# Kernel tuning notes

Measured on AMD Instinct MI355X. Metric: run time of the kernel, lower is better.

## Reference

```python
import jax, jax.numpy as jnp
import numpy as np

B, W, C, N = 2, 2048, 512, 8
K = C // N                      # 64
HALF = K * (K + 1) // 2 - K     # strict upper-triangle count
EPS = 1e-5


def _layernorm(x, gamma, beta):
    mu = jnp.mean(x, axis=-1, keepdims=True)
    var = jnp.mean(jnp.square(x - mu), axis=-1, keepdims=True)
    return (x - mu) * jax.lax.rsqrt(var + EPS) * gamma + beta


def _build_metric(halves, diagonals):
    # symmetric per-head metric: strict upper triangle from `halves`,
    # mirrored, diagonal overwritten by `diagonals` (diag of m+m^T is 0).
    iu0, iu1 = np.triu_indices(K, k=1)
    m = jnp.zeros((N, K, K), dtype=halves.dtype).at[:, iu0, iu1].set(halves)
    m = m + jnp.swapaxes(m, -1, -2)
    d = np.arange(K)
    return m.at[:, d, d].set(diagonals)


def setup_inputs() -> dict:
    key = jax.random.key(0)
    ks = jax.random.split(key, 9)
    return {
        "x1": jax.random.normal(ks[0], (B, W, C), jnp.float32),
        "x2": jax.random.normal(ks[1], (B, W, C), jnp.float32),
        "gamma": jnp.ones((C,), jnp.float32),
        "beta": jnp.zeros((C,), jnp.float32),
        "proj_nck": jax.random.normal(ks[2], (N, C, K), jnp.float32) * (C ** -0.5),
        "halves": jax.random.normal(ks[3], (N, HALF), jnp.float32) * 0.05,
        "diagonals": jax.random.normal(ks[4], (N, K), jnp.float32) * 0.05,
        "W_mixer": jax.random.normal(ks[5], (C, C), jnp.float32) * 0.02,
        "b_mixer": jnp.zeros((C,), jnp.float32),
    }


def reference(x1, x2, gamma, beta, proj_nck, halves, diagonals, W_mixer, b_mixer):
    x1n = _layernorm(x1, gamma, beta)
    x2n = _layernorm(x2, gamma, beta)
    metric_nkk = _build_metric(halves, diagonals)

    # per-head projections (same projection used for both sequences)
    p1_bnwk = jnp.einsum("bwc,nck->bnwk", x1n, proj_nck)
    p2_bnwk = jnp.einsum("bwc,nck->bnwk", x2n, proj_nck)

    # bilinear metric scores  Q . M . K^T  -> [B, N, W, W]
    dots_bnww = jnp.einsum("bnwk,nkj,bnvj->bnwv", p1_bnwk, metric_nkk, p2_bnwk)

    # NOTE: the original computes a scaled/masked softmax of dots_bnww but
    # never uses it for the output; the value mix uses the RAW dot products.
    # We omit the dead softmax — output math is identical.

    nudged_bnwk = jnp.einsum("bnwv,bnvk->bnwk", dots_bnww, p1_bnwk)
    nudged_bwc = jnp.transpose(nudged_bnwk, (0, 2, 1, 3)).reshape(x1.shape[0], x1.shape[1], C)
    return nudged_bwc @ W_mixer.T + b_mixer
```

## Files before the change

kernel.cpp:

```cpp
#include <hip/hip_runtime.h>

typedef unsigned short u16;
typedef __attribute__((ext_vector_type(8))) short short8;
typedef __attribute__((ext_vector_type(4))) float f32x4;

#define HALFN 2016

__device__ __forceinline__ u16 f2b_rn(float x) {
    union { float f; unsigned u; } v; v.f = x;
    unsigned r = v.u + 0x7FFFu + ((v.u >> 16) & 1u);
    return (u16)(r >> 16);
}

__device__ __forceinline__ void gll16(const void* g, void* s) {
    __builtin_amdgcn_global_load_lds(
        (const __attribute__((address_space(1))) unsigned int*)g,
        (__attribute__((address_space(3))) unsigned int*)s, 16, 0, 0);
}

__global__ __launch_bounds__(256) void ln_prep(const float* __restrict__ x1,
                                               const float* __restrict__ x2,
                                               const float* __restrict__ gamma,
                                               const float* __restrict__ beta,
                                               const float* __restrict__ proj,
                                               u16* __restrict__ Xh,
                                               u16* __restrict__ Pwh,
                                               float* __restrict__ S) {
    const int bid = blockIdx.x, t = threadIdx.x;

    if (bid < 2048) {
        const int wv = t >> 6, lane = t & 63;
        const int row = bid * 4 + wv;
        const float* src = (row < 4096) ? (x1 + (size_t)row * 512)
                                        : (x2 + (size_t)(row - 4096) * 512);
        float4 v0 = *(const float4*)&src[lane * 4];
        float4 v1 = *(const float4*)&src[256 + lane * 4];
        float s  = v0.x + v0.y + v0.z + v0.w + v1.x + v1.y + v1.z + v1.w;
        float sq = v0.x * v0.x + v0.y * v0.y + v0.z * v0.z + v0.w * v0.w +
                   v1.x * v1.x + v1.y * v1.y + v1.z * v1.z + v1.w * v1.w;
        #pragma unroll
        for (int off = 32; off > 0; off >>= 1) {
            s  += __shfl_down(s, off);
            sq += __shfl_down(sq, off);
        }
        s  = __shfl(s, 0);
        sq = __shfl(sq, 0);
        float mu  = s * (1.0f / 512.0f);
        float var = sq * (1.0f / 512.0f) - mu * mu;
        float rs  = rsqrtf(var + 1e-5f);
        float4 g0 = *(const float4*)&gamma[lane * 4];
        float4 g1 = *(const float4*)&gamma[256 + lane * 4];
        float4 b0 = *(const float4*)&beta[lane * 4];
        float4 b1 = *(const float4*)&beta[256 + lane * 4];
        ushort4 h0, h1;
        h0.x = f2b_rn((v0.x - mu) * rs * g0.x + b0.x);
        h0.y = f2b_rn((v0.y - mu) * rs * g0.y + b0.y);
        h0.z = f2b_rn((v0.z - mu) * rs * g0.z + b0.z);
        h0.w = f2b_rn((v0.w - mu) * rs * g0.w + b0.w);
        h1.x = f2b_rn((v1.x - mu) * rs * g1.x + b1.x);
        h1.y = f2b_rn((v1.y - mu) * rs * g1.y + b1.y);
        h1.z = f2b_rn((v1.z - mu) * rs * g1.z + b1.z);
        h1.w = f2b_rn((v1.w - mu) * rs * g1.w + b1.w);
        *(ushort4*)&Xh[(size_t)row * 512 + lane * 4] = h0;
        *(ushort4*)&Xh[(size_t)row * 512 + 256 + lane * 4] = h1;
    } else if (bid < 2112) {
        __shared__ float tile[64][65];
        const int id = bid - 2048;
        const int n = id >> 3, c0 = (id & 7) * 64;
        #pragma unroll
        for (int i = 0; i < 4; i++) {
            int flat = i * 256 + t;
            int c = flat >> 4, k4 = (flat & 15) * 4;
            float4 v = *(const float4*)&proj[(size_t)n * 32768 + (size_t)(c0 + c) * 64 + k4];
            tile[c][k4 + 0] = v.x; tile[c][k4 + 1] = v.y;
            tile[c][k4 + 2] = v.z; tile[c][k4 + 3] = v.w;
        }
        __syncthreads();
        #pragma unroll
        for (int i = 0; i < 16; i++) {
            int flat = i * 256 + t;
            int k = flat >> 6, c = flat & 63;
            Pwh[(size_t)(n * 64 + k) * 512 + c0 + c] = f2b_rn(tile[c][k]);
        }
    } else {
        float4 z = {0.f, 0.f, 0.f, 0.f};
        #pragma unroll
        for (int i = 0; i < 64; i++)
            *(float4*)&S[(size_t)(i * 256 + t) * 4] = z;
    }
}

template<int TM, int TN>
__device__ __forceinline__ void gemm_core_bk64(const u16* __restrict__ A,
                                               const u16* __restrict__ B,
                                               int m0, int n0, int ld, u16* lds,
                                               f32x4 (&acc)[TM / 32][TN / 32]) {
    constexpr int MI = TM / 32, NI = TN / 32;
    constexpr int LA = TM * 64;
    const int t = threadIdx.x;
    const int lane = t & 63;
    const int w = t >> 6, wm = w & 1, wn = w >> 1;
    const int fr = lane & 15, q = lane >> 4;

    int aoff[2][MI], boff[2][NI];
    #pragma unroll
    for (int kc = 0; kc < 2; kc++) {
        #pragma unroll
        for (int i = 0; i < MI; i++) {
            int r = wm * (TM / 2) + i * 16 + fr;
            aoff[kc][i] = r * 64 + (((kc * 4 + q) ^ (r & 7)) * 8);
        }
        #pragma unroll
        for (int j = 0; j < NI; j++) {
            int r = wn * (TN / 2) + j * 16 + fr;
            boff[kc][j] = r * 64 + (((kc * 4 + q) ^ (r & 7)) * 8);
        }
    }

    for (int kt = 0; kt < 512; kt += 64) {
        #pragma unroll
        for (int p = 0; p < TM / 32; p++) {
            int o = p * 4096 + t * 16;
            int r = o >> 7;
            int c = ((o >> 4) & 7) ^ (r & 7);
            gll16(A + (size_t)(m0 + r) * ld + kt + c * 8, lds + (o >> 1));
        }
        #pragma unroll
        for (int p = 0; p < TN / 32; p++) {
            int o = p * 4096 + t * 16;
            int r = o >> 7;
            int c = ((o >> 4) & 7) ^ (r & 7);
            gll16(B + (size_t)(n0 + r) * ld + kt + c * 8, lds + LA + (o >> 1));
        }
        __syncthreads();
        #pragma unroll
        for (int kc = 0; kc < 2; kc++) {
            short8 af[MI], bf[NI];
            #pragma unroll
            for (int i = 0; i < MI; i++)
                af[i] = *(const short8*)(lds + aoff[kc][i]);
            #pragma unroll
            for (int j = 0; j < NI; j++)
                bf[j] = *(const short8*)(lds + LA + boff[kc][j]);
            #pragma unroll
            for (int i = 0; i < MI; i++)
                #pragma unroll
                for (int j = 0; j < NI; j++)
                    acc[i][j] = __builtin_amdgcn_mfma_f32_16x16x32_bf16(af[i], bf[j], acc[i][j], 0, 0, 0);
        }
        __syncthreads();
    }
}

__global__ __launch_bounds__(256) void proj_g_mfma(const u16* __restrict__ Xh,
                                                   const u16* __restrict__ Pwh,
                                                   u16* __restrict__ PPh,
                                                   float* __restrict__ S) {
    __shared__ u16 lds[12288];
    const int bx = blockIdx.x;
    const int n  = blockIdx.y;
    const int b = bx >> 5, v0 = (bx & 31) * 64;
    const u16* A1 = Xh + (size_t)(b * 2048 + v0) * 512;
    const u16* A2 = A1 + (size_t)4096 * 512;
    const u16* Bp = Pwh + (size_t)(n * 64) * 512;

    const int t = threadIdx.x, lane = t & 63, w = t >> 6, wm = w & 1, wn = w >> 1;
    const int fr = lane & 15, q = lane >> 4;

    int aoff[2][2], boff[2][2];
    #pragma unroll
    for (int kc = 0; kc < 2; kc++) {
        #pragma unroll
        for (int i = 0; i < 2; i++) {
            int r = wm * 32 + i * 16 + fr;
            aoff[kc][i] = r * 64 + (((kc * 4 + q) ^ (r & 7)) * 8);
        }
        #pragma unroll
        for (int j = 0; j < 2; j++) {
            int r = wn * 32 + j * 16 + fr;
            boff[kc][j] = r * 64 + (((kc * 4 + q) ^ (r & 7)) * 8);
        }
    }

    f32x4 acc1[2][2] = {}, acc2[2][2] = {};
    const int o0 = t * 16;
    for (int kt = 0; kt < 512; kt += 64) {
        #pragma unroll
        for (int p = 0; p < 2; p++) {
            int o = p * 4096 + o0;
            int r = o >> 7;
            int c = ((o >> 4) & 7) ^ (r & 7);
            size_t g = (size_t)r * 512 + kt + c * 8;
            gll16(A1 + g, lds + (o >> 1));
            gll16(A2 + g, lds + 4096 + (o >> 1));
            gll16(Bp + g, lds + 8192 + (o >> 1));
        }
        __syncthreads();
        #pragma unroll
        for (int kc = 0; kc < 2; kc++) {
            short8 a1f[2], a2f[2], bf[2];
            #pragma unroll
            for (int i = 0; i < 2; i++) {
                a1f[i] = *(const short8*)(lds + aoff[kc][i]);
                a2f[i] = *(const short8*)(lds + 4096 + aoff[kc][i]);
            }
            #pragma unroll
            for (int j = 0; j < 2; j++)
                bf[j] = *(const short8*)(lds + 8192 + boff[kc][j]);
            #pragma unroll
            for (int i = 0; i < 2; i++)
                #pragma unroll
                for (int j = 0; j < 2; j++) {
                    acc1[i][j] = __builtin_amdgcn_mfma_f32_16x16x32_bf16(a1f[i], bf[j], acc1[i][j], 0, 0, 0);
                    acc2[i][j] = __builtin_amdgcn_mfma_f32_16x16x32_bf16(a2f[i], bf[j], acc2[i][j], 0, 0, 0);
                }
        }
        __syncthreads();
    }

    #pragma unroll
    for (int i = 0; i < 2; i++) {
        const int mloc = wm * 32 + i * 16 + q * 4;
        #pragma unroll
        for (int j = 0; j < 2; j++) {
            const int c = wn * 32 + j * 16 + fr;
            u16 h1[4], h2[4];
            #pragma unroll
            for (int r = 0; r < 4; r++) {
                h1[r] = f2b_rn(acc1[i][j][r]);
                h2[r] = f2b_rn(acc2[i][j][r]);
            }
            #pragma unroll
            for (int r = 0; r < 4; r++)
                PPh[(size_t)(b * 2048 + v0 + mloc + r) * 512 + n * 64 + c] = h1[r];
            const int sw = c * 64 + (((mloc >> 3) ^ (c & 7)) * 8) + (mloc & 7);
            ushort4 u1; u1.x = h1[0]; u1.y = h1[1]; u1.z = h1[2]; u1.w = h1[3];
            ushort4 u2; u2.x = h2[0]; u2.y = h2[1]; u2.z = h2[2]; u2.w = h2[3];
            *(ushort4*)&lds[sw] = u1;
            *(ushort4*)&lds[4096 + sw] = u2;
        }
    }
    __syncthreads();

    f32x4 accg[2][2] = {};
    #pragma unroll
    for (int ks = 0; ks < 2; ks++) {
        short8 ag[2], bg[2];
        #pragma unroll
        for (int i = 0; i < 2; i++) {
            int jr = wm * 32 + i * 16 + fr;
            ag[i] = *(const short8*)&lds[4096 + jr * 64 + (((ks * 4 + q) ^ (jr & 7)) * 8)];
        }
        #pragma unroll
        for (int j = 0; j < 2; j++) {
            int kr = wn * 32 + j * 16 + fr;
            bg[j] = *(const short8*)&lds[kr * 64 + (((ks * 4 + q) ^ (kr & 7)) * 8)];
        }
        #pragma unroll
        for (int i = 0; i < 2; i++)
            #pragma unroll
            for (int j = 0; j < 2; j++)
                accg[i][j] = __builtin_amdgcn_mfma_f32_16x16x32_bf16(ag[i], bg[j], accg[i][j], 0, 0, 0);
    }
    float* Sb = S + (size_t)(b * 8 + n) * 4096;
    #pragma unroll
    for (int i = 0; i < 2; i++) {
        int jrow = wm * 32 + i * 16 + q * 4;
        #pragma unroll
        for (int j = 0; j < 2; j++) {
            int kk = wn * 32 + j * 16 + fr;
            #pragma unroll
            for (int r = 0; r < 4; r++)
                atomicAdd(&Sb[(jrow + r) * 64 + kk], accg[i][j][r]);
        }
    }
}

__global__ __launch_bounds__(256) void tu_kernel(const float* __restrict__ S,
                                                 const float* __restrict__ halves,
                                                 const float* __restrict__ diagonals,
                                                 const float* __restrict__ Wm,
                                                 u16* __restrict__ UTh) {
    __shared__ float Ms[64][65];
    __shared__ float Gs[64][68];
    __shared__ float Ts[64][68];
    const int bid = blockIdx.x, t = threadIdx.x;
    const int bn = bid >> 3, b = bn >> 3, n = bn & 7, cy = bid & 7;

    for (int idx = t; idx < 4096; idx += 256) {
        int r = idx >> 6, c = idx & 63;
        float val;
        if (r == c) {
            val = diagonals[n * 64 + r];
        } else {
            int rr = (r < c) ? r : c;
            int cc = (r < c) ? c : r;
            int h = rr * 63 - (rr * (rr - 1)) / 2 + (cc - rr - 1);
            val = halves[n * HALFN + h];
        }
        Ms[r][c] = val;
    }
    for (int idx = t; idx < 4096; idx += 256)
        Gs[idx >> 6][idx & 63] = S[(size_t)bn * 4096 + idx];
    __syncthreads();

    {
        const int k = t & 63, lq = t >> 6;
        float a[16] = {};
        for (int j = 0; j < 64; j++) {
            float m = Ms[k][j];
            const float* gp = &Gs[j][lq * 16];
            #pragma unroll
            for (int u4 = 0; u4 < 4; u4++) {
                float4 g4 = *(const float4*)&gp[u4 * 4];
                a[u4 * 4 + 0] = fmaf(m, g4.x, a[u4 * 4 + 0]);
                a[u4 * 4 + 1] = fmaf(m, g4.y, a[u4 * 4 + 1]);
                a[u4 * 4 + 2] = fmaf(m, g4.z, a[u4 * 4 + 2]);
                a[u4 * 4 + 3] = fmaf(m, g4.w, a[u4 * 4 + 3]);
            }
        }
        int pos = (lq ^ (k & 3)) * 16;
        #pragma unroll
        for (int u4 = 0; u4 < 4; u4++) {
            float4 v4 = {a[u4 * 4 + 0], a[u4 * 4 + 1], a[u4 * 4 + 2], a[u4 * 4 + 3]};
            *(float4*)&Ts[k][pos + u4 * 4] = v4;
        }
    }
    __syncthreads();

    const int k2 = t & 63, cgp = t >> 6;
    const int c0 = cy * 64 + cgp * 16;
    float uacc[16] = {};
    #pragma unroll
    for (int kkc = 0; kkc < 4; kkc++) {
        const float* tp = &Ts[k2][(kkc ^ (k2 & 3)) * 16];
        float ts[16];
        #pragma unroll
        for (int u = 0; u < 4; u++) {
            float4 t4 = *(const float4*)&tp[u * 4];
            ts[u * 4 + 0] = t4.x; ts[u * 4 + 1] = t4.y;
            ts[u * 4 + 2] = t4.z; ts[u * 4 + 3] = t4.w;
        }
        #pragma unroll
        for (int i = 0; i < 16; i++) {
            const float* wrow = &Wm[(size_t)(c0 + i) * 512 + n * 64 + kkc * 16];
            #pragma unroll
            for (int u = 0; u < 4; u++) {
                float4 w4 = *(const float4*)&wrow[u * 4];
                uacc[i] = fmaf(ts[u * 4 + 0], w4.x, uacc[i]);
                uacc[i] = fmaf(ts[u * 4 + 1], w4.y, uacc[i]);
                uacc[i] = fmaf(ts[u * 4 + 2], w4.z, uacc[i]);
                uacc[i] = fmaf(ts[u * 4 + 3], w4.w, uacc[i]);
            }
        }
    }
    #pragma unroll
    for (int i = 0; i < 16; i++)
        UTh[(size_t)b * 262144 + (size_t)(c0 + i) * 512 + n * 64 + k2] = f2b_rn(uacc[i]);
}

__global__ __launch_bounds__(256) void gemm_out_mfma(const u16* __restrict__ PPh,
                                                     const u16* __restrict__ UTh,
                                                     const float* __restrict__ bias,
                                                     float* __restrict__ out) {
    __shared__ u16 lds[8192];
    const int b = blockIdx.z;
    const u16* A = PPh + (size_t)b * 2048 * 512;
    const u16* B = UTh + (size_t)b * 512 * 512;
    f32x4 acc[2][2] = {};
    const int m0 = blockIdx.x * 64, n0 = blockIdx.y * 64;
    gemm_core_bk64<64, 64>(A, B, m0, n0, 512, lds, acc);
    const int t = threadIdx.x, lane = t & 63, w = t >> 6, wm = w & 1, wn = w >> 1;
    const int fr = lane & 15, q = lane >> 4;
    #pragma unroll
    for (int i = 0; i < 2; i++) {
        int m = m0 + wm * 32 + i * 16 + q * 4;
        #pragma unroll
        for (int j = 0; j < 2; j++) {
            int n = n0 + wn * 32 + j * 16 + fr;
            float bv = bias[n];
            #pragma unroll
            for (int r = 0; r < 4; r++)
                out[(size_t)(b * 2048 + m + r) * 512 + n] = acc[i][j][r] + bv;
        }
    }
}

extern "C" void kernel_launch(void* const* d_in, const int* in_sizes, int n_in,
                              void* d_out, int out_size, void* d_ws, size_t ws_size,
                              hipStream_t stream) {
    (void)in_sizes; (void)n_in; (void)out_size; (void)ws_size;
    const float* x1        = (const float*)d_in[0];
    const float* x2        = (const float*)d_in[1];
    const float* gamma     = (const float*)d_in[2];
    const float* beta      = (const float*)d_in[3];
    const float* proj      = (const float*)d_in[4];
    const float* halves    = (const float*)d_in[5];
    const float* diagonals = (const float*)d_in[6];
    const float* Wm        = (const float*)d_in[7];
    const float* bmix      = (const float*)d_in[8];
    float* out = (float*)d_out;

    u16* us    = (u16*)d_ws;
    u16* Xh    = us;
    u16* Pwh   = Xh + 4194304;
    u16* PPh   = Pwh + 262144;
    u16* UTh   = PPh + 2097152;
    float* S   = (float*)(UTh + 524288);

    ln_prep<<<dim3(2113), 256, 0, stream>>>(x1, x2, gamma, beta, proj, Xh, Pwh, S);
    proj_g_mfma<<<dim3(64, 8), 256, 0, stream>>>(Xh, Pwh, PPh, S);
    tu_kernel<<<dim3(128), 256, 0, stream>>>(S, halves, diagonals, Wm, UTh);
    gemm_out_mfma<<<dim3(32, 8, 2), 256, 0, stream>>>(PPh, UTh, bmix, out);
}
```

Measured before the change: 121.1 us.

## Double-buffer LDS in projection and output GEMMs; split tu_kernel over more blocks

The projection and output GEMMs now use two LDS buffers, so the global-to-LDS loads for the next K tile are issued before the MFMAs on the current tile run. This removes one barrier per iteration and is meant to hide load latency. tu_kernel goes from 128 to 512 blocks, each computing 4 output columns per thread instead of 16, to fill more CUs. The cost is recomputing the per-block G/T setup four times as often and doubling LDS use, which may lower occupancy.

```diff
diff --git a/kernel.cpp b/kernel.cpp
--- a/kernel.cpp
+++ b/kernel.cpp
@@ -90,73 +90,11 @@
     }
 }
 
-template<int TM, int TN>
-__device__ __forceinline__ void gemm_core_bk64(const u16* __restrict__ A,
-                                               const u16* __restrict__ B,
-                                               int m0, int n0, int ld, u16* lds,
-                                               f32x4 (&acc)[TM / 32][TN / 32]) {
-    constexpr int MI = TM / 32, NI = TN / 32;
-    constexpr int LA = TM * 64;
-    const int t = threadIdx.x;
-    const int lane = t & 63;
-    const int w = t >> 6, wm = w & 1, wn = w >> 1;
-    const int fr = lane & 15, q = lane >> 4;
-
-    int aoff[2][MI], boff[2][NI];
-    #pragma unroll
-    for (int kc = 0; kc < 2; kc++) {
-        #pragma unroll
-        for (int i = 0; i < MI; i++) {
-            int r = wm * (TM / 2) + i * 16 + fr;
-            aoff[kc][i] = r * 64 + (((kc * 4 + q) ^ (r & 7)) * 8);
-        }
-        #pragma unroll
-        for (int j = 0; j < NI; j++) {
-            int r = wn * (TN / 2) + j * 16 + fr;
-            boff[kc][j] = r * 64 + (((kc * 4 + q) ^ (r & 7)) * 8);
-        }
-    }
-
-    for (int kt = 0; kt < 512; kt += 64) {
-        #pragma unroll
-        for (int p = 0; p < TM / 32; p++) {
-            int o = p * 4096 + t * 16;
-            int r = o >> 7;
-            int c = ((o >> 4) & 7) ^ (r & 7);
-            gll16(A + (size_t)(m0 + r) * ld + kt + c * 8, lds + (o >> 1));
-        }
-        #pragma unroll
-        for (int p = 0; p < TN / 32; p++) {
-            int o = p * 4096 + t * 16;
-            int r = o >> 7;
-            int c = ((o >> 4) & 7) ^ (r & 7);
-            gll16(B + (size_t)(n0 + r) * ld + kt + c * 8, lds + LA + (o >> 1));
-        }
-        __syncthreads();
-        #pragma unroll
-        for (int kc = 0; kc < 2; kc++) {
-            short8 af[MI], bf[NI];
-            #pragma unroll
-            for (int i = 0; i < MI; i++)
-                af[i] = *(const short8*)(lds + aoff[kc][i]);
-            #pragma unroll
-            for (int j = 0; j < NI; j++)
-                bf[j] = *(const short8*)(lds + LA + boff[kc][j]);
-            #pragma unroll
-            for (int i = 0; i < MI; i++)
-                #pragma unroll
-                for (int j = 0; j < NI; j++)
-                    acc[i][j] = __builtin_amdgcn_mfma_f32_16x16x32_bf16(af[i], bf[j], acc[i][j], 0, 0, 0);
-        }
-        __syncthreads();
-    }
-}
-
 __global__ __launch_bounds__(256) void proj_g_mfma(const u16* __restrict__ Xh,
                                                    const u16* __restrict__ Pwh,
                                                    u16* __restrict__ PPh,
                                                    float* __restrict__ S) {
-    __shared__ u16 lds[12288];
+    __shared__ u16 lds[24576];
     const int bx = blockIdx.x;
     const int n  = blockIdx.y;
     const int b = bx >> 5, v0 = (bx & 31) * 64;
@@ -182,31 +120,36 @@
         }
     }
 
-    f32x4 acc1[2][2] = {}, acc2[2][2] = {};
-    const int o0 = t * 16;
-    for (int kt = 0; kt < 512; kt += 64) {
+    auto stage = [&](int kt, u16* buf) {
         #pragma unroll
         for (int p = 0; p < 2; p++) {
-            int o = p * 4096 + o0;
+            int o = p * 4096 + t * 16;
             int r = o >> 7;
             int c = ((o >> 4) & 7) ^ (r & 7);
             size_t g = (size_t)r * 512 + kt + c * 8;
-            gll16(A1 + g, lds + (o >> 1));
-            gll16(A2 + g, lds + 4096 + (o >> 1));
-            gll16(Bp + g, lds + 8192 + (o >> 1));
-        }
-        __syncthreads();
+            gll16(A1 + g, buf + (o >> 1));
+            gll16(A2 + g, buf + 4096 + (o >> 1));
+            gll16(Bp + g, buf + 8192 + (o >> 1));
+        }
+    };
+
+    f32x4 acc1[2][2] = {}, acc2[2][2] = {};
+    stage(0, lds);
+    __syncthreads();
+    for (int k = 0; k < 8; k++) {
+        u16* cur = lds + (k & 1) * 12288;
+        if (k < 7) stage((k + 1) * 64, lds + ((k & 1) ^ 1) * 12288);
         #pragma unroll
         for (int kc = 0; kc < 2; kc++) {
             short8 a1f[2], a2f[2], bf[2];
             #pragma unroll
             for (int i = 0; i < 2; i++) {
-                a1f[i] = *(const short8*)(lds + aoff[kc][i]);
-                a2f[i] = *(const short8*)(lds + 4096 + aoff[kc][i]);
+                a1f[i] = *(const short8*)(cur + aoff[kc][i]);
+                a2f[i] = *(const short8*)(cur + 4096 + aoff[kc][i]);
             }
             #pragma unroll
             for (int j = 0; j < 2; j++)
-                bf[j] = *(const short8*)(lds + 8192 + boff[kc][j]);
+                bf[j] = *(const short8*)(cur + 8192 + boff[kc][j]);
             #pragma unroll
             for (int i = 0; i < 2; i++)
                 #pragma unroll
@@ -285,7 +228,8 @@
     __shared__ float Gs[64][68];
     __shared__ float Ts[64][68];
     const int bid = blockIdx.x, t = threadIdx.x;
-    const int bn = bid >> 3, b = bn >> 3, n = bn & 7, cy = bid & 7;
+    const int bn = bid >> 5, sub = bid & 31;
+    const int b = bn >> 3, n = bn & 7;
 
     for (int idx = t; idx < 4096; idx += 256) {
         int r = idx >> 6, c = idx & 63;
@@ -329,8 +273,8 @@
     __syncthreads();
 
     const int k2 = t & 63, cgp = t >> 6;
-    const int c0 = cy * 64 + cgp * 16;
-    float uacc[16] = {};
+    const int c0 = sub * 16 + cgp * 4;
+    float uacc[4] = {};
     #pragma unroll
     for (int kkc = 0; kkc < 4; kkc++) {
         const float* tp = &Ts[k2][(kkc ^ (k2 & 3)) * 16];
@@ -342,7 +286,7 @@
             ts[u * 4 + 2] = t4.z; ts[u * 4 + 3] = t4.w;
         }
         #pragma unroll
-        for (int i = 0; i < 16; i++) {
+        for (int i = 0; i < 4; i++) {
             const float* wrow = &Wm[(size_t)(c0 + i) * 512 + n * 64 + kkc * 16];
             #pragma unroll
             for (int u = 0; u < 4; u++) {
@@ -355,7 +299,7 @@
         }
     }
     #pragma unroll
-    for (int i = 0; i < 16; i++)
+    for (int i = 0; i < 4; i++)
         UTh[(size_t)b * 262144 + (size_t)(c0 + i) * 512 + n * 64 + k2] = f2b_rn(uacc[i]);
 }
 
@@ -363,15 +307,64 @@
                                                      const u16* __restrict__ UTh,
                                                      const float* __restrict__ bias,
                                                      float* __restrict__ out) {
-    __shared__ u16 lds[8192];
+    __shared__ u16 lds[16384];
     const int b = blockIdx.z;
-    const u16* A = PPh + (size_t)b * 2048 * 512;
-    const u16* B = UTh + (size_t)b * 512 * 512;
-    f32x4 acc[2][2] = {};
+    const u16* A  = PPh + (size_t)b * 2048 * 512;
+    const u16* Bu = UTh + (size_t)b * 512 * 512;
     const int m0 = blockIdx.x * 64, n0 = blockIdx.y * 64;
-    gemm_core_bk64<64, 64>(A, B, m0, n0, 512, lds, acc);
     const int t = threadIdx.x, lane = t & 63, w = t >> 6, wm = w & 1, wn = w >> 1;
     const int fr = lane & 15, q = lane >> 4;
+
+    int aoff[2][2], boff[2][2];
+    #pragma unroll
+    for (int kc = 0; kc < 2; kc++) {
+        #pragma unroll
+        for (int i = 0; i < 2; i++) {
+            int r = wm * 32 + i * 16 + fr;
+            aoff[kc][i] = r * 64 + (((kc * 4 + q) ^ (r & 7)) * 8);
+        }
+        #pragma unroll
+        for (int j = 0; j < 2; j++) {
+            int r = wn * 32 + j * 16 + fr;
+            boff[kc][j] = r * 64 + (((kc * 4 + q) ^ (r & 7)) * 8);
+        }
+    }
+
+    auto stage = [&](int kt, u16* buf) {
+        #pragma unroll
+        for (int p = 0; p < 2; p++) {
+            int o = p * 4096 + t * 16;
+            int r = o >> 7;
+            int c = ((o >> 4) & 7) ^ (r & 7);
+            gll16(A  + (size_t)(m0 + r) * 512 + kt + c * 8, buf + (o >> 1));
+            gll16(Bu + (size_t)(n0 + r) * 512 + kt + c * 8, buf + 4096 + (o >> 1));
+        }
+    };
+
+    f32x4 acc[2][2] = {};
+    stage(0, lds);
+    __syncthreads();
+    for (int k = 0; k < 8; k++) {
+        u16* cur = lds + (k & 1) * 8192;
+        if (k < 7) stage((k + 1) * 64, lds + ((k & 1) ^ 1) * 8192);
+        #pragma unroll
+        for (int kc = 0; kc < 2; kc++) {
+            short8 af[2], bf[2];
+            #pragma unroll
+            for (int i = 0; i < 2; i++)
+                af[i] = *(const short8*)(cur + aoff[kc][i]);
+            #pragma unroll
+            for (int j = 0; j < 2; j++)
+                bf[j] = *(const short8*)(cur + 4096 + boff[kc][j]);
+            #pragma unroll
+            for (int i = 0; i < 2; i++)
+                #pragma unroll
+                for (int j = 0; j < 2; j++)
+                    acc[i][j] = __builtin_amdgcn_mfma_f32_16x16x32_bf16(af[i], bf[j], acc[i][j], 0, 0, 0);
+        }
+        __syncthreads();
+    }
+
     #pragma unroll
     for (int i = 0; i < 2; i++) {
         int m = m0 + wm * 32 + i * 16 + q * 4;
@@ -410,6 +403,6 @@
 
     ln_prep<<<dim3(2113), 256, 0, stream>>>(x1, x2, gamma, beta, proj, Xh, Pwh, S);
     proj_g_mfma<<<dim3(64, 8), 256, 0, stream>>>(Xh, Pwh, PPh, S);
-    tu_kernel<<<dim3(128), 256, 0, stream>>>(S, halves, diagonals, Wm, UTh);
+    tu_kernel<<<dim3(512), 256, 0, stream>>>(S, halves, diagonals, Wm, UTh);
     gemm_out_mfma<<<dim3(32, 8, 2), 256, 0, stream>>>(PPh, UTh, bmix, out);
 }
```

Measured after the change: 116.7 us. 3.7% less time.
